# Kernel optimization log

Measured on AMD Instinct MI355X. Metric: run time of the kernel, lower is better.

The kernel has to match this reference:

```python
import jax, jax.numpy as jnp
import numpy as np

B, S, D, H = 2, 2048, 2048, 16
HD = D // H  # 128
ROPE_BASE = 10000.0


def _rope_tables(seq_len, head_dim, dtype=jnp.float32):
    inv_freq = 1.0 / (ROPE_BASE ** (jnp.arange(0, head_dim, 2, dtype=jnp.float32) / head_dim))
    t = jnp.arange(seq_len, dtype=jnp.float32)
    freqs = jnp.outer(t, inv_freq)  # [S, HD/2]
    # broadcast shape [1, S, 1, HD/2]
    return jnp.cos(freqs)[None, :, None, :].astype(dtype), jnp.sin(freqs)[None, :, None, :].astype(dtype)


def _apply_rope(x, cos, sin):
    # x: [B, S, H, HD]; interleaved split, output concatenated by halves (matches torch code)
    x1 = x[..., ::2]
    x2 = x[..., 1::2]
    return jnp.concatenate([x1 * cos - x2 * sin, x1 * sin + x2 * cos], axis=-1)


def setup_inputs() -> dict:
    key = jax.random.key(0)
    ks = jax.random.split(key, 9)
    xavier = lambda k: jax.random.uniform(k, (D, D), jnp.float32, -1.0, 1.0) * np.sqrt(6.0 / (D + D))
    return {
        "x": jax.random.normal(ks[0], (B, S, D), jnp.float32),
        "attention_mask": jnp.ones((B, S), jnp.int32),
        "wq": xavier(ks[1]), "bq": jnp.zeros((D,), jnp.float32),
        "wk": xavier(ks[2]), "bk": jnp.zeros((D,), jnp.float32),
        "wv": xavier(ks[3]), "bv": jnp.zeros((D,), jnp.float32),
        "wo": xavier(ks[4]), "bo": jnp.zeros((D,), jnp.float32),
    }


def reference(x, attention_mask, wq, bq, wk, bk, wv, bv, wo, bo):
    b, s, _ = x.shape
    scale = HD ** -0.5
    q = (x @ wq + bq).reshape(b, s, H, HD)
    k = (x @ wk + bk).reshape(b, s, H, HD)
    v = (x @ wv + bv).reshape(b, s, H, HD)
    cos, sin = _rope_tables(s, HD, x.dtype)
    q = _apply_rope(q, cos, sin)
    k = _apply_rope(k, cos, sin)
    # [B, H, S, S]
    scores = jnp.einsum('bqhd,bkhd->bhqk', q, k) * scale
    mask = attention_mask[:, None, None, :]  # 2D mask -> [B,1,1,S]
    scores = jnp.where(mask == 0, jnp.asarray(-1e9, scores.dtype), scores)
    attn = jax.nn.softmax(scores, axis=-1)
    out = jnp.einsum('bhqk,bkhd->bqhd', attn, v).reshape(b, s, D)
    return out @ wo + bo
```

## Files before the change

kernel.cpp:

```cpp
#include <hip/hip_runtime.h>

#define Bc 2
#define Sc 2048
#define Dc 2048
#define Hc 16
#define HDc 128
#define Mc 4096

typedef __bf16 bf16_t;
typedef __bf16 bf16x4 __attribute__((ext_vector_type(4)));
typedef __bf16 bf16x8 __attribute__((ext_vector_type(8)));
typedef float f32x4 __attribute__((ext_vector_type(4)));
typedef float f32x16 __attribute__((ext_vector_type(16)));

__device__ __forceinline__ f32x4 mfma16(bf16x8 a, bf16x8 b, f32x4 c) {
  return __builtin_amdgcn_mfma_f32_16x16x32_bf16(a, b, c, 0, 0, 0);
}
__device__ __forceinline__ f32x16 mfma32(bf16x8 a, bf16x8 b, f32x16 c) {
  return __builtin_amdgcn_mfma_f32_32x32x16_bf16(a, b, c, 0, 0, 0);
}

typedef const unsigned __attribute__((address_space(1))) gu32_t;
typedef unsigned __attribute__((address_space(3))) lu32_t;

__device__ __forceinline__ void gload_lds16(const void* g, void* l) {
  gu32_t* gp = (gu32_t*)(unsigned long long)g;
  lu32_t* lp = (lu32_t*)(unsigned)(unsigned long long)l;
  __builtin_amdgcn_global_load_lds(gp, lp, 16, 0, 0);
}

__device__ __forceinline__ unsigned cvtpk(float lo, float hi_) {
  unsigned r;
  asm("v_cvt_pk_bf16_f32 %0, %1, %2" : "=v"(r) : "v"(lo), "v"(hi_));
  return r;
}
__device__ __forceinline__ void plswap(unsigned& a, unsigned& b) {
  asm volatile("v_permlane32_swap_b32 %0, %1" : "+v"(a), "+v"(b));
}
__device__ __forceinline__ float fexp2(float x) {
  float r;
  asm("v_exp_f32 %0, %1" : "=v"(r) : "v"(x));
  return r;
}

__global__ void cvt_bf16_kernel(const float* __restrict__ in, bf16_t* __restrict__ out, int n4) {
  int i = blockIdx.x * blockDim.x + threadIdx.x;
  if (i < n4) {
    float4 v = ((const float4*)in)[i];
    bf16x4 o;
    o[0] = (bf16_t)v.x; o[1] = (bf16_t)v.y; o[2] = (bf16_t)v.z; o[3] = (bf16_t)v.w;
    ((bf16x4*)out)[i] = o;
  }
}

__global__ void rope_table_kernel(float2* __restrict__ tbl) {
  const int s = blockIdx.x, j = threadIdx.x;
  float freq = expf(-(float)j * (9.210340371976184f / 64.0f));
  float ang = (float)s * freq;
  float sn, cs;
  sincosf(ang, &sn, &cs);
  tbl[s * 64 + j] = make_float2(cs, sn);
}

__global__ void transpose_cvt4_kernel(const float* __restrict__ w0, const float* __restrict__ w1,
                                      const float* __restrict__ w2, const float* __restrict__ w3,
                                      bf16_t* __restrict__ dqkv, bf16_t* __restrict__ dwo) {
  __shared__ float tile[32][33];
  const int z = blockIdx.z;
  const float* w = z == 0 ? w0 : (z == 1 ? w1 : (z == 2 ? w2 : w3));
  bf16_t* wt = z < 3 ? dqkv + (size_t)z * Dc * Dc : dwo;
  const int tx = threadIdx.x, ty = threadIdx.y;
  const int n0 = blockIdx.x * 32, k0 = blockIdx.y * 32;
#pragma unroll
  for (int i = 0; i < 32; i += 8)
    tile[ty + i][tx] = w[(size_t)(k0 + ty + i) * Dc + n0 + tx];
  __syncthreads();
#pragma unroll
  for (int i = 0; i < 32; i += 8)
    wt[(size_t)(n0 + ty + i) * Dc + k0 + tx] = (bf16_t)tile[tx][ty + i];
}

template <int MODE, int NT8>
__global__ __launch_bounds__(512, 1) void gemmp_kernel(
    const bf16_t* __restrict__ A, const bf16_t* __restrict__ Bt,
    const float* __restrict__ bias0, const float* __restrict__ bias1,
    const float* __restrict__ bias2, const float2* __restrict__ tbl,
    void* __restrict__ out0, void* __restrict__ out1, void* __restrict__ out2) {
  __shared__ __align__(16) bf16_t sA[3][256 * 64];
  __shared__ __align__(16) bf16_t sB[3][128 * 64];
  const int tid = threadIdx.x;
  const int lane = tid & 63, wid = tid >> 6;
  const int l15 = lane & 15, g = lane >> 4;
  const int wrow = wid >> 1, wcol = wid & 1;

  const int nwg = 16 * NT8, cpx = nwg / 8;
  const int wgid = ((int)blockIdx.x & 7) * cpx + ((int)blockIdx.x >> 3);
  const int nt = wgid % NT8, mt = wgid / NT8;
  const int m0 = mt * 256, n0 = nt * 128;

  const bf16_t* Ab = A + (size_t)m0 * 2048;
  const bf16_t* Bb = Bt + (size_t)n0 * 2048;

#define GP_STAGE_A(kt, i_)                                           \
  {                                                                  \
    int s_ = (i_) * 512 + tid;                                       \
    int r_ = s_ >> 3;                                                \
    int c_ = ((s_ & 7) ^ (r_ & 7)) * 8;                              \
    gload_lds16(Ab + (size_t)r_ * 2048 + (kt) * 64 + c_,             \
                (char*)&sA[(kt) % 3][0] + s_ * 16);                  \
  }
#define GP_STAGE_B(kt, i_)                                           \
  {                                                                  \
    int s_ = (i_) * 512 + tid;                                       \
    int r_ = s_ >> 3;                                                \
    int c_ = ((s_ & 7) ^ (r_ & 7)) * 8;                              \
    gload_lds16(Bb + (size_t)r_ * 2048 + (kt) * 64 + c_,             \
                (char*)&sB[(kt) % 3][0] + s_ * 16);                  \
  }

  f32x4 acc[4][4] = {};

  GP_STAGE_A(0, 0) GP_STAGE_A(0, 1) GP_STAGE_A(0, 2) GP_STAGE_A(0, 3)
  GP_STAGE_B(0, 0) GP_STAGE_B(0, 1)
  GP_STAGE_A(1, 0) GP_STAGE_A(1, 1) GP_STAGE_A(1, 2) GP_STAGE_A(1, 3)
  GP_STAGE_B(1, 0) GP_STAGE_B(1, 1)

#define GP_BODY(t, DOSTG, VMSTR)                                               \
  {                                                                            \
    asm volatile("s_waitcnt vmcnt(" VMSTR ")" ::: "memory");                   \
    __builtin_amdgcn_s_barrier();                                              \
    __builtin_amdgcn_sched_barrier(0);                                         \
    const char* pA = (const char*)&sA[(t) % 3][0];                             \
    const char* pB = (const char*)&sB[(t) % 3][0];                             \
    bf16x8 af[4][2], bf0[2][2], bf1[2][2];                                     \
    _Pragma("unroll") for (int mi = 0; mi < 4; ++mi)                           \
        _Pragma("unroll") for (int ks = 0; ks < 2; ++ks) {                     \
      int r = wrow * 64 + mi * 16 + l15;                                       \
      af[mi][ks] = *(const bf16x8*)(pA + r * 128 + (((ks * 4 + g) ^ (r & 7)) * 16)); \
    }                                                                          \
    _Pragma("unroll") for (int ni = 0; ni < 2; ++ni)                           \
        _Pragma("unroll") for (int ks = 0; ks < 2; ++ks) {                     \
      int r = wcol * 64 + ni * 16 + l15;                                       \
      bf0[ni][ks] = *(const bf16x8*)(pB + r * 128 + (((ks * 4 + g) ^ (r & 7)) * 16)); \
    }                                                                          \
    if (DOSTG) { GP_STAGE_A((t) + 2, 0) GP_STAGE_A((t) + 2, 1) GP_STAGE_B((t) + 2, 0) } \
    __builtin_amdgcn_s_setprio(1);                                             \
    _Pragma("unroll") for (int mi = 0; mi < 4; ++mi)                           \
        _Pragma("unroll") for (int ni = 0; ni < 2; ++ni)                       \
            _Pragma("unroll") for (int ks = 0; ks < 2; ++ks)                   \
                acc[mi][ni] = mfma16(af[mi][ks], bf0[ni][ks], acc[mi][ni]);    \
    __builtin_amdgcn_s_setprio(0);                                             \
    __builtin_amdgcn_s_barrier();                                              \
    __builtin_amdgcn_sched_barrier(0);                                         \
    _Pragma("unroll") for (int ni = 0; ni < 2; ++ni)                           \
        _Pragma("unroll") for (int ks = 0; ks < 2; ++ks) {                     \
      int r = wcol * 64 + (ni + 2) * 16 + l15;                                 \
      bf1[ni][ks] = *(const bf16x8*)(pB + r * 128 + (((ks * 4 + g) ^ (r & 7)) * 16)); \
    }                                                                          \
    if (DOSTG) { GP_STAGE_A((t) + 2, 2) GP_STAGE_A((t) + 2, 3) GP_STAGE_B((t) + 2, 1) } \
    __builtin_amdgcn_s_setprio(1);                                             \
    _Pragma("unroll") for (int mi = 0; mi < 4; ++mi)                           \
        _Pragma("unroll") for (int ni = 0; ni < 2; ++ni)                       \
            _Pragma("unroll") for (int ks = 0; ks < 2; ++ks)                   \
                acc[mi][ni + 2] = mfma16(af[mi][ks], bf1[ni][ks], acc[mi][ni + 2]); \
    __builtin_amdgcn_s_setprio(0);                                             \
  }

  for (int t = 0; t < 30; ++t) GP_BODY(t, 1, "6");
  GP_BODY(30, 0, "6");
  GP_BODY(31, 0, "0");

#undef GP_BODY
#undef GP_STAGE_A
#undef GP_STAGE_B

  if (MODE == 2) {
#pragma unroll
    for (int mi = 0; mi < 4; ++mi) {
#pragma unroll
      for (int ni = 0; ni < 4; ++ni) {
        const int ncol = n0 + wcol * 64 + ni * 16 + l15;
        const float bv = bias0[ncol];
#pragma unroll
        for (int r = 0; r < 4; ++r) {
          const int mrow = m0 + wrow * 64 + mi * 16 + g * 4 + r;
          ((float*)out0)[(size_t)mrow * 2048 + ncol] = acc[mi][ni][r] + bv;
        }
      }
    }
  } else {
    const int proj = n0 >> 11;
    const float* bp = proj == 0 ? bias0 : (proj == 1 ? bias1 : bias2);
    bf16_t* op = (bf16_t*)(proj == 0 ? out0 : (proj == 1 ? out1 : out2));
#pragma unroll
    for (int mi = 0; mi < 4; ++mi) {
#pragma unroll
      for (int ni = 0; ni < 4; ++ni) {
        const int ncol = n0 + wcol * 64 + ni * 16 + l15;
        const int nloc = ncol & 2047;
        const float bv = bp[nloc];
        const int h = nloc >> 7, hd = nloc & 127;
        if (proj < 2) {
          const int j = hd >> 1;
#pragma unroll
          for (int r = 0; r < 4; ++r) {
            const int mrow = m0 + wrow * 64 + mi * 16 + g * 4 + r;
            const int b = mrow >> 11, sq = mrow & 2047;
            float vv = acc[mi][ni][r] + bv;
            float part = __shfl_xor(vv, 1);
            float2 cn = tbl[(size_t)sq * 64 + j];
            float ov = (l15 & 1) ? (part * cn.y + vv * cn.x)
                                 : (vv * cn.x - part * cn.y);
            op[(((size_t)(b * Hc + h) * Sc + sq) * HDc) + hd] = (bf16_t)ov;
          }
        } else {
#pragma unroll
          for (int r = 0; r < 4; ++r) {
            const int mrow = m0 + wrow * 64 + mi * 16 + g * 4 + r;
            const int b = mrow >> 11, sq = mrow & 2047;
            const float v = acc[mi][ni][r] + bv;
            op[(((size_t)(b * Hc + h) * HDc + hd) * Sc) + sq] = (bf16_t)v;
          }
        }
      }
    }
  }
}

__global__ __launch_bounds__(256, 2) void attn_kernel(
    const bf16_t* __restrict__ Q, const bf16_t* __restrict__ Kr,
    const bf16_t* __restrict__ Vt, const int* __restrict__ mask,
    bf16_t* __restrict__ AO) {
  __shared__ __align__(16) bf16_t sK[2][64 * 128];
  __shared__ __align__(16) bf16_t sV[2][64 * 128];
  __shared__ float mbias[Sc];
  __shared__ float bcast[4][32];
  const int tid = threadIdx.x;
  const int w = tid >> 6, lane = tid & 63;
  const int l31 = lane & 31, hi = lane >> 5;
  const int wbase = w * 64;

  const int bid = blockIdx.x;
  const int L = ((bid & 7) << 6) + (bid >> 3);
  const int qc = L & 15, h = (L >> 4) & 15, b = L >> 8;

  const int* mb = mask + b * Sc;
#pragma unroll
  for (int i = 0; i < Sc / 256; ++i)
    mbias[i * 256 + tid] = mb[i * 256 + tid] ? 0.f : -1.4426950408889634e9f;

  const int q0 = qc * 128 + w * 32;
  const bf16_t* qb = Q + ((size_t)(b * Hc + h) * Sc + q0) * HDc;
  const bf16_t* kb = Kr + ((size_t)(b * Hc + h) * Sc) * HDc;
  const bf16_t* vb = Vt + ((size_t)(b * Hc + h) * HDc) * Sc;

  bf16x8 qf[8];
  {
    const bf16_t* qr = qb + (size_t)l31 * HDc + hi * 8;
#pragma unroll
    for (int kk = 0; kk < 8; ++kk) qf[kk] = *(const bf16x8*)(qr + kk * 16);
  }

#define STAGE_KV(sKb, sVb, kv0_)                                             \
  {                                                                          \
    _Pragma("unroll") for (int p = 0; p < 4; ++p) {                          \
      int s_ = p * 256 + tid;                                                \
      int rk = s_ >> 4, ck = s_ & 15;                                        \
      gload_lds16(kb + (size_t)((kv0_) + rk) * HDc + ((ck ^ (rk & 15)) * 8), \
                  (char*)(sKb) + (size_t)(p * 256 + wbase) * 16);            \
      int d63 = s_ >> 4, sv = s_ & 15;                                       \
      int tmp = sv ^ (d63 & 15);                                             \
      int hb = tmp >> 3, cv = tmp & 7;                                       \
      gload_lds16(vb + (size_t)(hb * 64 + d63) * Sc + (kv0_) + cv * 8,       \
                  (char*)(sVb) + (size_t)(p * 256 + wbase) * 16);            \
    }                                                                        \
  }

  bf16_t* sKc = &sK[0][0];
  bf16_t* sKn = &sK[1][0];
  bf16_t* sVc = &sV[0][0];
  bf16_t* sVn = &sV[1][0];

  STAGE_KV(sKc, sVc, 0);
  asm volatile("s_waitcnt vmcnt(0)" ::: "memory");
  __syncthreads();

  f32x16 acc[4];
#pragma unroll
  for (int d = 0; d < 4; ++d) acc[d] = 0.f;
  float mrun = -3.0e38f, lrun = 0.f;
  const float scale2 = 0.12751744f;

  for (int kv0 = 0; kv0 < Sc; kv0 += 64) {
    if (kv0 + 64 < Sc) STAGE_KV(sKn, sVn, kv0 + 64);

    f32x16 s0 = 0.f, s1 = 0.f;
    {
      const char* kbase = (const char*)sKc;
      __builtin_amdgcn_s_setprio(1);
#pragma unroll
      for (int kk = 0; kk < 8; ++kk) {
        bf16x8 k0f = *(const bf16x8*)(kbase + l31 * 256 + (((2 * kk + hi) ^ (l31 & 15)) * 16));
        bf16x8 k1f = *(const bf16x8*)(kbase + (32 + l31) * 256 + (((2 * kk + hi) ^ ((32 + l31) & 15)) * 16));
        s0 = mfma32(k0f, qf[kk], s0);
        s1 = mfma32(k1f, qf[kk], s1);
      }
      __builtin_amdgcn_s_setprio(0);
    }
    float v[32];
    {
      const float* mp = mbias + kv0 + 4 * hi;
#pragma unroll
      for (int g4 = 0; g4 < 4; ++g4) {
        f32x4 b0 = *(const f32x4*)(mp + 8 * g4);
        f32x4 b1 = *(const f32x4*)(mp + 32 + 8 * g4);
#pragma unroll
        for (int j = 0; j < 4; ++j) {
          v[g4 * 4 + j] = s0[g4 * 4 + j] * scale2 + b0[j];
          v[16 + g4 * 4 + j] = s1[g4 * 4 + j] * scale2 + b1[j];
        }
      }
    }
    float t16[16];
#pragma unroll
    for (int r = 0; r < 16; ++r) t16[r] = fmaxf(v[r], v[r + 16]);
#pragma unroll
    for (int r = 0; r < 8; ++r) t16[r] = fmaxf(t16[r], t16[r + 8]);
#pragma unroll
    for (int r = 0; r < 4; ++r) t16[r] = fmaxf(t16[r], t16[r + 4]);
    float tm = fmaxf(fmaxf(t16[0], t16[1]), fmaxf(t16[2], t16[3]));
    tm = fmaxf(tm, __shfl_xor(tm, 32));
    if (__any(tm > mrun + 11.5415603f)) {
      float mnew = fmaxf(mrun, tm);
      float al = fexp2(mrun - mnew);
      mrun = mnew;
      lrun *= al;
      bcast[w][l31] = al;
      asm volatile("s_waitcnt lgkmcnt(0)" ::: "memory");
      __builtin_amdgcn_sched_barrier(0);
#pragma unroll
      for (int g4 = 0; g4 < 4; ++g4) {
        f32x4 alr = *(const f32x4*)(&bcast[w][8 * g4 + 4 * hi]);
#pragma unroll
        for (int dblk = 0; dblk < 4; ++dblk)
#pragma unroll
          for (int j = 0; j < 4; ++j) acc[dblk][g4 * 4 + j] *= alr[j];
      }
    }
    float ts = 0.f;
#pragma unroll
    for (int r = 0; r < 32; ++r) {
      v[r] = fexp2(v[r] - mrun);
      ts += v[r];
    }
    ts += __shfl_xor(ts, 32);
    lrun += ts;
    unsigned pk[4][4];
#pragma unroll
    for (int ks = 0; ks < 4; ++ks) {
      unsigned a1 = cvtpk(v[ks * 8 + 0], v[ks * 8 + 1]);
      unsigned b1 = cvtpk(v[ks * 8 + 4], v[ks * 8 + 5]);
      unsigned a2 = cvtpk(v[ks * 8 + 2], v[ks * 8 + 3]);
      unsigned b2 = cvtpk(v[ks * 8 + 6], v[ks * 8 + 7]);
      plswap(a1, b1);
      plswap(a2, b2);
      pk[ks][0] = a1; pk[ks][1] = a2; pk[ks][2] = b1; pk[ks][3] = b2;
    }
    {
      const char* vbase = (const char*)sVc;
      __builtin_amdgcn_s_setprio(1);
#pragma unroll
      for (int ks = 0; ks < 4; ++ks) {
        bf16x8 pa = *(const bf16x8*)&pk[ks][0];
#pragma unroll
        for (int dblk = 0; dblk < 4; ++dblk) {
          int d = dblk * 32 + l31;
          int slot = (((d >> 6) * 8 + (2 * ks + hi)) ^ (d & 15));
          bf16x8 vf = *(const bf16x8*)(vbase + (d & 63) * 256 + slot * 16);
          acc[dblk] = mfma32(pa, vf, acc[dblk]);
        }
      }
      __builtin_amdgcn_s_setprio(0);
    }
    asm volatile("s_waitcnt vmcnt(0)" ::: "memory");
    __syncthreads();
    bf16_t* t1 = sKc; sKc = sKn; sKn = t1;
    bf16_t* t2 = sVc; sVc = sVn; sVn = t2;
  }

  float inv = 1.f / lrun;
  bcast[w][l31] = inv;
  asm volatile("s_waitcnt lgkmcnt(0)" ::: "memory");
  __builtin_amdgcn_sched_barrier(0);
  bf16_t* ob = AO + ((size_t)b * Sc + q0) * Dc + h * HDc;
#pragma unroll
  for (int g4 = 0; g4 < 4; ++g4) {
    f32x4 ir = *(const f32x4*)(&bcast[w][8 * g4 + 4 * hi]);
#pragma unroll
    for (int j = 0; j < 4; ++j) {
      int q = 8 * g4 + 4 * hi + j;
#pragma unroll
      for (int dblk = 0; dblk < 4; ++dblk)
        ob[(size_t)q * Dc + dblk * 32 + l31] = (bf16_t)(acc[dblk][g4 * 4 + j] * ir[j]);
    }
  }
}

#define MB(x) ((size_t)(x) << 20)

extern "C" void kernel_launch(void* const* d_in, const int* in_sizes, int n_in,
                              void* d_out, int out_size, void* d_ws, size_t ws_size,
                              hipStream_t stream) {
  const float* x = (const float*)d_in[0];
  const int* mask = (const int*)d_in[1];
  const float* wq = (const float*)d_in[2];
  const float* bq = (const float*)d_in[3];
  const float* wk = (const float*)d_in[4];
  const float* bk = (const float*)d_in[5];
  const float* wv = (const float*)d_in[6];
  const float* bv = (const float*)d_in[7];
  const float* wo = (const float*)d_in[8];
  const float* bo = (const float*)d_in[9];
  float* out = (float*)d_out;

  char* ws = (char*)d_ws;
  bf16_t* xb     = (bf16_t*)(ws + MB(0));
  bf16_t* wqkvT  = (bf16_t*)(ws + MB(16));
  bf16_t* woT    = (bf16_t*)(ws + MB(40));
  bf16_t* qbuf   = (bf16_t*)(ws + MB(48));
  bf16_t* kbuf   = (bf16_t*)(ws + MB(64));
  bf16_t* vtb    = (bf16_t*)(ws + MB(80));
  bf16_t* ao     = (bf16_t*)(ws + MB(96));
  float2* rtbl   = (float2*)(ws + MB(112));

  cvt_bf16_kernel<<<8192, 256, 0, stream>>>(x, xb, (Mc * Dc) / 4);
  rope_table_kernel<<<Sc, 64, 0, stream>>>(rtbl);

  dim3 tg(64, 64, 4), tb(32, 8);
  transpose_cvt4_kernel<<<tg, tb, 0, stream>>>(wq, wk, wv, wo, wqkvT, woT);

  gemmp_kernel<0, 48><<<768, 512, 0, stream>>>(xb, wqkvT, bq, bk, bv, rtbl, qbuf, kbuf, vtb);

  attn_kernel<<<Bc * Hc * (Sc / 128), 256, 0, stream>>>(qbuf, kbuf, vtb, mask, ao);

  gemmp_kernel<2, 16><<<256, 512, 0, stream>>>(ao, woT, bo, bo, bo, rtbl, out, out, out);
}
```

Measured before the change: 266.4 us.

## Use 256x256-tile double-buffered GEMM for fused QKV projection

Adds a new QKV projection kernel that uses 256x256 output tiles with a 2-stage LDS double buffer and 8 waves laid out 2x4, where each wave computes 128x64. This halves the number of workgroups (384 instead of 768) and raises arithmetic intensity per LDS byte loaded. The cost is a shallower pipeline (2 stages instead of 3, with a full vmcnt(0) wait each iteration), a heavier register load from 32 accumulators per lane, and 384 tiles over 256 CUs, which is a worse wave-quantization tail. The output projection GEMM is simplified to a single-mode kernel.

```diff
diff --git a/kernel.cpp b/kernel.cpp
--- a/kernel.cpp
+++ b/kernel.cpp
@@ -80,12 +80,123 @@
     wt[(size_t)(n0 + ty + i) * Dc + k0 + tx] = (bf16_t)tile[tx][ty + i];
 }
 
-template <int MODE, int NT8>
-__global__ __launch_bounds__(512, 1) void gemmp_kernel(
+template <int NT>
+__global__ __launch_bounds__(512, 1) void gemmq_kernel(
     const bf16_t* __restrict__ A, const bf16_t* __restrict__ Bt,
     const float* __restrict__ bias0, const float* __restrict__ bias1,
     const float* __restrict__ bias2, const float2* __restrict__ tbl,
     void* __restrict__ out0, void* __restrict__ out1, void* __restrict__ out2) {
+  __shared__ __align__(16) bf16_t sA[2][256 * 64];
+  __shared__ __align__(16) bf16_t sB[2][256 * 64];
+  const int tid = threadIdx.x;
+  const int lane = tid & 63, wid = tid >> 6;
+  const int l15 = lane & 15, g = lane >> 4;
+  const int wr = wid >> 2, wc = wid & 3;
+
+  const int nwg = 16 * NT, cpx = nwg / 8;
+  const int wgid = ((int)blockIdx.x & 7) * cpx + ((int)blockIdx.x >> 3);
+  const int nt = wgid % NT, mt = wgid / NT;
+  const int m0 = mt * 256, n0 = nt * 256;
+
+  const bf16_t* Ab = A + (size_t)m0 * 2048;
+  const bf16_t* Bb = Bt + (size_t)n0 * 2048;
+
+#define GQ_STAGE(kt)                                                  \
+  {                                                                   \
+    const int sl_ = (kt) & 1;                                         \
+    _Pragma("unroll") for (int i_ = 0; i_ < 4; ++i_) {                \
+      int s_ = i_ * 512 + tid;                                        \
+      int r_ = s_ >> 3;                                               \
+      int c_ = ((s_ & 7) ^ (r_ & 7)) * 8;                             \
+      gload_lds16(Ab + (size_t)r_ * 2048 + (kt) * 64 + c_,            \
+                  (char*)&sA[sl_][0] + s_ * 16);                      \
+    }                                                                 \
+    _Pragma("unroll") for (int i_ = 0; i_ < 4; ++i_) {                \
+      int s_ = i_ * 512 + tid;                                        \
+      int r_ = s_ >> 3;                                               \
+      int c_ = ((s_ & 7) ^ (r_ & 7)) * 8;                             \
+      gload_lds16(Bb + (size_t)r_ * 2048 + (kt) * 64 + c_,            \
+                  (char*)&sB[sl_][0] + s_ * 16);                      \
+    }                                                                 \
+  }
+
+  f32x4 acc[8][4] = {};
+
+  GQ_STAGE(0);
+
+  for (int t = 0; t < 32; ++t) {
+    asm volatile("s_waitcnt vmcnt(0)" ::: "memory");
+    __builtin_amdgcn_s_barrier();
+    __builtin_amdgcn_sched_barrier(0);
+    if (t < 31) GQ_STAGE(t + 1);
+    const char* pA = (const char*)&sA[t & 1][0];
+    const char* pB = (const char*)&sB[t & 1][0];
+#pragma unroll
+    for (int ks = 0; ks < 2; ++ks) {
+      bf16x8 af[8], bfr[4];
+#pragma unroll
+      for (int mi = 0; mi < 8; ++mi) {
+        int r = wr * 128 + mi * 16 + l15;
+        af[mi] = *(const bf16x8*)(pA + r * 128 + (((ks * 4 + g) ^ (r & 7)) * 16));
+      }
+#pragma unroll
+      for (int ni = 0; ni < 4; ++ni) {
+        int r = wc * 64 + ni * 16 + l15;
+        bfr[ni] = *(const bf16x8*)(pB + r * 128 + (((ks * 4 + g) ^ (r & 7)) * 16));
+      }
+      __builtin_amdgcn_s_setprio(1);
+#pragma unroll
+      for (int mi = 0; mi < 8; ++mi)
+#pragma unroll
+        for (int ni = 0; ni < 4; ++ni)
+          acc[mi][ni] = mfma16(af[mi], bfr[ni], acc[mi][ni]);
+      __builtin_amdgcn_s_setprio(0);
+    }
+  }
+
+#undef GQ_STAGE
+
+  const int proj = n0 >> 11;
+  const float* bp = proj == 0 ? bias0 : (proj == 1 ? bias1 : bias2);
+  bf16_t* op = (bf16_t*)(proj == 0 ? out0 : (proj == 1 ? out1 : out2));
+#pragma unroll
+  for (int mi = 0; mi < 8; ++mi) {
+#pragma unroll
+    for (int ni = 0; ni < 4; ++ni) {
+      const int ncol = n0 + wc * 64 + ni * 16 + l15;
+      const int nloc = ncol & 2047;
+      const float bv = bp[nloc];
+      const int h = nloc >> 7, hd = nloc & 127;
+      if (proj < 2) {
+        const int j = hd >> 1;
+#pragma unroll
+        for (int r = 0; r < 4; ++r) {
+          const int mrow = m0 + wr * 128 + mi * 16 + g * 4 + r;
+          const int b = mrow >> 11, sq = mrow & 2047;
+          float vv = acc[mi][ni][r] + bv;
+          float part = __shfl_xor(vv, 1);
+          float2 cn = tbl[(size_t)sq * 64 + j];
+          float ov = (l15 & 1) ? (part * cn.y + vv * cn.x)
+                               : (vv * cn.x - part * cn.y);
+          op[(((size_t)(b * Hc + h) * Sc + sq) * HDc) + hd] = (bf16_t)ov;
+        }
+      } else {
+#pragma unroll
+        for (int r = 0; r < 4; ++r) {
+          const int mrow = m0 + wr * 128 + mi * 16 + g * 4 + r;
+          const int b = mrow >> 11, sq = mrow & 2047;
+          const float v = acc[mi][ni][r] + bv;
+          op[(((size_t)(b * Hc + h) * HDc + hd) * Sc) + sq] = (bf16_t)v;
+        }
+      }
+    }
+  }
+}
+
+template <int NT8>
+__global__ __launch_bounds__(512, 1) void gemmp_kernel(
+    const bf16_t* __restrict__ A, const bf16_t* __restrict__ Bt,
+    const float* __restrict__ bias0, void* __restrict__ out0) {
   __shared__ __align__(16) bf16_t sA[3][256 * 64];
   __shared__ __align__(16) bf16_t sB[3][128 * 64];
   const int tid = threadIdx.x;
@@ -174,54 +285,16 @@
 #undef GP_STAGE_A
 #undef GP_STAGE_B
 
-  if (MODE == 2) {
-#pragma unroll
-    for (int mi = 0; mi < 4; ++mi) {
-#pragma unroll
-      for (int ni = 0; ni < 4; ++ni) {
-        const int ncol = n0 + wcol * 64 + ni * 16 + l15;
-        const float bv = bias0[ncol];
-#pragma unroll
-        for (int r = 0; r < 4; ++r) {
-          const int mrow = m0 + wrow * 64 + mi * 16 + g * 4 + r;
-          ((float*)out0)[(size_t)mrow * 2048 + ncol] = acc[mi][ni][r] + bv;
-        }
-      }
-    }
-  } else {
-    const int proj = n0 >> 11;
-    const float* bp = proj == 0 ? bias0 : (proj == 1 ? bias1 : bias2);
-    bf16_t* op = (bf16_t*)(proj == 0 ? out0 : (proj == 1 ? out1 : out2));
-#pragma unroll
-    for (int mi = 0; mi < 4; ++mi) {
-#pragma unroll
-      for (int ni = 0; ni < 4; ++ni) {
-        const int ncol = n0 + wcol * 64 + ni * 16 + l15;
-        const int nloc = ncol & 2047;
-        const float bv = bp[nloc];
-        const int h = nloc >> 7, hd = nloc & 127;
-        if (proj < 2) {
-          const int j = hd >> 1;
-#pragma unroll
-          for (int r = 0; r < 4; ++r) {
-            const int mrow = m0 + wrow * 64 + mi * 16 + g * 4 + r;
-            const int b = mrow >> 11, sq = mrow & 2047;
-            float vv = acc[mi][ni][r] + bv;
-            float part = __shfl_xor(vv, 1);
-            float2 cn = tbl[(size_t)sq * 64 + j];
-            float ov = (l15 & 1) ? (part * cn.y + vv * cn.x)
-                                 : (vv * cn.x - part * cn.y);
-            op[(((size_t)(b * Hc + h) * Sc + sq) * HDc) + hd] = (bf16_t)ov;
-          }
-        } else {
-#pragma unroll
-          for (int r = 0; r < 4; ++r) {
-            const int mrow = m0 + wrow * 64 + mi * 16 + g * 4 + r;
-            const int b = mrow >> 11, sq = mrow & 2047;
-            const float v = acc[mi][ni][r] + bv;
-            op[(((size_t)(b * Hc + h) * HDc + hd) * Sc) + sq] = (bf16_t)v;
-          }
-        }
+#pragma unroll
+  for (int mi = 0; mi < 4; ++mi) {
+#pragma unroll
+    for (int ni = 0; ni < 4; ++ni) {
+      const int ncol = n0 + wcol * 64 + ni * 16 + l15;
+      const float bv = bias0[ncol];
+#pragma unroll
+      for (int r = 0; r < 4; ++r) {
+        const int mrow = m0 + wrow * 64 + mi * 16 + g * 4 + r;
+        ((float*)out0)[(size_t)mrow * 2048 + ncol] = acc[mi][ni][r] + bv;
       }
     }
   }
@@ -439,9 +512,9 @@
   dim3 tg(64, 64, 4), tb(32, 8);
   transpose_cvt4_kernel<<<tg, tb, 0, stream>>>(wq, wk, wv, wo, wqkvT, woT);
 
-  gemmp_kernel<0, 48><<<768, 512, 0, stream>>>(xb, wqkvT, bq, bk, bv, rtbl, qbuf, kbuf, vtb);
+  gemmq_kernel<24><<<384, 512, 0, stream>>>(xb, wqkvT, bq, bk, bv, rtbl, qbuf, kbuf, vtb);
 
   attn_kernel<<<Bc * Hc * (Sc / 128), 256, 0, stream>>>(qbuf, kbuf, vtb, mask, ao);
 
-  gemmp_kernel<2, 16><<<256, 512, 0, stream>>>(ao, woT, bo, bo, bo, rtbl, out, out, out);
-}
+  gemmp_kernel<16><<<256, 512, 0, stream>>>(ao, woT, bo, out);
+}
```

Measured after the change: 280.0 us. 5.1% more time.
